# Performance work log

Hardware: AMD Instinct MI355X
Metric: run time of the kernel (lower is better)

The kernel has to match this reference:

```python
import jax, jax.numpy as jnp
import numpy as np


def setup_inputs() -> dict:
    key = jax.random.key(0)
    ks = jax.random.split(key, 6)
    B, N, d = 4096, 32768, 512
    return {
        "X_src": jax.random.normal(ks[0], (B, d), dtype=jnp.float32),
        "X_trans": jax.random.normal(ks[1], (B, d), dtype=jnp.float32),
        "Y_tgt": jax.random.normal(ks[2], (B, d), dtype=jnp.float32),
        "Z_src": jax.random.normal(ks[3], (N, d), dtype=jnp.float32),
        "Z_trans": jax.random.normal(ks[4], (N, d), dtype=jnp.float32),
        "Z_tgt": jax.random.normal(ks[5], (N, d), dtype=jnp.float32),
        "knn": 10,
    }


def _getknn(sc, k):
    # torch: topk(10) indices[:, :k], gather, sum  ==  sum of top-k values per row
    vals, _ = jax.lax.top_k(sc, k)  # [rows, k]
    return vals.sum() / k


def reference(X_src, X_trans, Y_tgt, Z_src, Z_trans, Z_tgt, knn):
    B = X_src.shape[0]
    f = 2.0 * (X_trans * Y_tgt).sum()
    # sc0: [B, N] similarity of translated src words vs target vocab
    fk0 = _getknn(X_trans @ Z_tgt.T, knn)
    # Z_trans.mm(Y_tgt.t()).t() == Y_tgt @ Z_trans.T : [B, N]
    fk1 = _getknn(Y_tgt @ Z_trans.T, knn)
    f = f - fk0 - fk1
    return -f / B
```

## Files before the change

kernel.cpp:

```cpp
#include <hip/hip_runtime.h>
#include <hip/hip_bf16.h>
#include <float.h>
#include <cstdint>


#define B_ROWS 4096
#define N_COLS 32768
#define D_K    512
#define BM     128
#define BN     128
#define BKT    64
#define NCHUNK (N_COLS / BN)
#define CSTRIDE 134

typedef __bf16 bf16x8 __attribute__((ext_vector_type(8)));
typedef float  f32x4  __attribute__((ext_vector_type(4)));
typedef unsigned short u16x2 __attribute__((ext_vector_type(2)));

__device__ __forceinline__ unsigned short f2bf(float f) {
    unsigned int u = __float_as_uint(f);
    u += 0x7FFFu + ((u >> 16) & 1u);
    return (unsigned short)(u >> 16);
}
__device__ __forceinline__ unsigned short f2sort(float f) {
    unsigned int x = f2bf(f);
    return (unsigned short)(x ^ (0x8000u | ((x >> 15) * 0x7FFFu)));
}
__device__ __forceinline__ float sort2f(unsigned int y) {
    unsigned int x = (y & 0x8000u) ? (y ^ 0x8000u) : (~y & 0xFFFFu);
    return __uint_as_float(x << 16);
}

__device__ __forceinline__ void gload_lds16(const void* g, void* l) {
    __builtin_amdgcn_global_load_lds(
        (const __attribute__((address_space(1))) unsigned int*)(uintptr_t)g,
        (__attribute__((address_space(3))) unsigned int*)(uintptr_t)l,
        16, 0, 0);
}

__global__ void zero_scalars(float* sc) {
    if (threadIdx.x < 3) sc[threadIdx.x] = 0.0f;
}

__global__ void prep_kernel(const float4* __restrict__ X,
                            const float4* __restrict__ Y,
                            const float4* __restrict__ Zt,
                            const float4* __restrict__ Ztr,
                            ushort4* __restrict__ A0, ushort4* __restrict__ A1,
                            ushort4* __restrict__ B0, ushort4* __restrict__ B1,
                            float* __restrict__ dotacc) {
    const int z = blockIdx.y;
    int i = blockIdx.x * 256 + threadIdx.x;
    const int stride = gridDim.x * 256;
    if (z == 0) {
        float s = 0.0f;
        for (; i < B_ROWS * D_K / 4; i += stride) {
            float4 x = X[i], y = Y[i];
            ushort4 u; u.x = f2bf(x.x); u.y = f2bf(x.y);
            u.z = f2bf(x.z); u.w = f2bf(x.w);
            A0[i] = u;
            s += x.x * y.x + x.y * y.y + x.z * y.z + x.w * y.w;
        }
        for (int o = 32; o > 0; o >>= 1) s += __shfl_down(s, o);
        __shared__ float wsum[4];
        int lane = threadIdx.x & 63, w = threadIdx.x >> 6;
        if (lane == 0) wsum[w] = s;
        __syncthreads();
        if (threadIdx.x == 0)
            atomicAdd(dotacc, wsum[0] + wsum[1] + wsum[2] + wsum[3]);
    } else {
        const float4* src = (z == 1) ? Y : (z == 2) ? Zt : Ztr;
        ushort4* dst = (z == 1) ? A1 : (z == 2) ? B0 : B1;
        int n4 = (z == 1) ? (B_ROWS * D_K / 4) : (N_COLS * D_K / 4);
        for (; i < n4; i += stride) {
            float4 f = src[i];
            ushort4 u; u.x = f2bf(f.x); u.y = f2bf(f.y);
            u.z = f2bf(f.z); u.w = f2bf(f.w);
            dst[i] = u;
        }
    }
}

__global__ __launch_bounds__(256, 4)
void gemm_topk_kernel(const unsigned short* __restrict__ A0g,
                      const unsigned short* __restrict__ A1g,
                      const unsigned short* __restrict__ B0g,
                      const unsigned short* __restrict__ B1g,
                      uint2* __restrict__ P0, uint2* __restrict__ P1) {
    const unsigned short* A  = blockIdx.y ? A1g : A0g;
    const unsigned short* Bm = blockIdx.y ? B1g : B0g;
    uint2* P2 = blockIdx.y ? P1 : P0;

    __shared__ __align__(128) unsigned short smem[BM * CSTRIDE];
    unsigned short* Alds = smem;
    unsigned short* Blds = smem + 16 * 512;

    const int tid  = threadIdx.x;
    const int lane = tid & 63;
    const int w    = tid >> 6;
    const int wm   = w >> 1;
    const int wn   = w & 1;
    const int quad = lane >> 4;
    const int mrow = lane & 15;

    const int b      = blockIdx.x;
    const int xcd    = b & 7;
    const int ii     = b >> 3;
    const int cw     = ii & 15;
    const int rowblk = (ii >> 4) & 31;
    const int cg     = ii >> 9;
    const int bn     = xcd * 32 + cg * 16 + cw;
    const int row0   = rowblk * BM;
    const int col0   = bn * BN;

    const unsigned short* gA[4];
    const unsigned short* gB[4];
    #pragma unroll
    for (int c = 0; c < 4; ++c) {
        int s  = w * 4 + c;
        int r  = (s >> 1) * 16 + mrow;
        int kc = (s & 1) * 32 + quad * 8;
        gA[c] = A  + (size_t)(row0 + r) * D_K + kc;
        gB[c] = Bm + (size_t)(col0 + r) * D_K + kc;
    }

    f32x4 acc[4][4];
    #pragma unroll
    for (int mi = 0; mi < 4; ++mi)
        #pragma unroll
        for (int ni = 0; ni < 4; ++ni)
            acc[mi][ni] = (f32x4){0.f, 0.f, 0.f, 0.f};

    for (int kt = 0; kt < D_K; kt += BKT) {
        #pragma unroll
        for (int c = 0; c < 4; ++c) {
            int s = w * 4 + c;
            gload_lds16(gA[c] + kt, Alds + s * 512);
            gload_lds16(gB[c] + kt, Blds + s * 512);
        }
        __syncthreads();
        #pragma unroll
        for (int kk32 = 0; kk32 < 2; ++kk32) {
            bf16x8 af[4], bfr[4];
            #pragma unroll
            for (int mi = 0; mi < 4; ++mi)
                af[mi] = *(const bf16x8*)(Alds + ((wm * 4 + mi) * 2 + kk32) * 512 + lane * 8);
            #pragma unroll
            for (int ni = 0; ni < 4; ++ni)
                bfr[ni] = *(const bf16x8*)(Blds + ((wn * 4 + ni) * 2 + kk32) * 512 + lane * 8);
            #pragma unroll
            for (int mi = 0; mi < 4; ++mi)
                #pragma unroll
                for (int ni = 0; ni < 4; ++ni)
                    acc[mi][ni] = __builtin_amdgcn_mfma_f32_16x16x32_bf16(
                        af[mi], bfr[ni], acc[mi][ni], 0, 0, 0);
        }
        __syncthreads();
    }

    unsigned short* Cs = smem;
    #pragma unroll
    for (int mi = 0; mi < 4; ++mi) {
        int r = wm * 64 + mi * 16 + quad * 4;
        #pragma unroll
        for (int ni = 0; ni < 4; ++ni) {
            int cc = wn * 64 + ni * 16 + mrow;
            #pragma unroll
            for (int reg = 0; reg < 4; ++reg)
                Cs[(r + reg) * CSTRIDE + cc] = f2sort(acc[mi][ni][reg]);
        }
    }
    __syncthreads();

    const int row  = w * 32 + (lane >> 1);
    const int half = lane & 1;
    const u16x2* rp = (const u16x2*)(Cs + row * CSTRIDE + half * 64);
    u16x2 t[4];
    #pragma unroll
    for (int i = 0; i < 4; ++i) t[i] = (u16x2){0, 0};
    #pragma unroll 8
    for (int j = 0; j < 32; ++j) {
        u16x2 v = rp[j];
        #pragma unroll
        for (int i = 0; i < 4; ++i) {
            u16x2 hi = __builtin_elementwise_max(t[i], v);
            v = __builtin_elementwise_min(t[i], v);
            t[i] = hi;
        }
    }
    unsigned int m0 = max((unsigned int)t[0].x, (unsigned int)t[3].y);
    unsigned int m1 = max((unsigned int)t[1].x, (unsigned int)t[2].y);
    unsigned int m2 = max((unsigned int)t[2].x, (unsigned int)t[1].y);
    unsigned int m3 = max((unsigned int)t[3].x, (unsigned int)t[0].y);
    uint2 outv = make_uint2(m0 | (m1 << 16), m2 | (m3 << 16));
    P2[((size_t)(row0 + row) * NCHUNK + bn) * 2 + half] = outv;
}

__global__ __launch_bounds__(256, 4)
void merge_topk_kernel(const unsigned int* __restrict__ P0,
                       const unsigned int* __restrict__ P1,
                       float* __restrict__ sc) {
    const int g    = blockIdx.y;
    const int lane = threadIdx.x & 63;
    const int w    = threadIdx.x >> 6;
    const int row  = blockIdx.x * 4 + w;
    const unsigned int* Rp = (g ? P1 : P0) + (size_t)row * (NCHUNK * 4);

    u16x2 t[10];
    #pragma unroll
    for (int i = 0; i < 10; ++i) t[i] = (u16x2){0, 0};
    #pragma unroll 4
    for (int it = 0; it < 16; ++it) {
        unsigned int raw = Rp[lane + 64 * it];
        u16x2 v = *(u16x2*)&raw;
        #pragma unroll
        for (int i = 0; i < 10; ++i) {
            u16x2 hi = __builtin_elementwise_max(t[i], v);
            v = __builtin_elementwise_min(t[i], v);
            t[i] = hi;
        }
    }
    unsigned int wreg[10];
    #pragma unroll
    for (int i = 0; i < 10; ++i) {
        unsigned int mv = max((unsigned int)t[i].x,
                              (unsigned int)t[9 - i].y);
        wreg[i] = (mv << 16) | ((unsigned int)lane << 4) | (unsigned int)i;
    }
    float sum10 = 0.0f;
    #pragma unroll
    for (int iter = 0; iter < 10; ++iter) {
        unsigned int mx = wreg[0];
        #pragma unroll
        for (int s = 1; s < 10; ++s) mx = max(mx, wreg[s]);
        #pragma unroll
        for (int o = 32; o > 0; o >>= 1)
            mx = max(mx, (unsigned int)__shfl_xor((int)mx, o));
        sum10 += sort2f(mx >> 16);
        #pragma unroll
        for (int s = 0; s < 10; ++s)
            if (wreg[s] == mx) wreg[s] = 0u;
    }
    if (lane == 0) atomicAdd(sc + 1 + g, sum10);
}

__global__ void finalize_kernel(const float* __restrict__ sc,
                                float* __restrict__ out) {
    if (threadIdx.x == 0) {
        float f = (sc[1] * 0.1f + sc[2] * 0.1f - 2.0f * sc[0]) * (1.0f / 4096.0f);
        out[0] = f;
    }
}

extern "C" void kernel_launch(void* const* d_in, const int* in_sizes, int n_in,
                              void* d_out, int out_size, void* d_ws, size_t ws_size,
                              hipStream_t stream) {
    const float* X_trans = (const float*)d_in[1];
    const float* Y_tgt   = (const float*)d_in[2];
    const float* Z_trans = (const float*)d_in[4];
    const float* Z_tgt   = (const float*)d_in[5];

    char* ws = (char*)d_ws;
    float* sc = (float*)ws;
    unsigned short* A0 = (unsigned short*)(ws + 256);
    unsigned short* A1 = A0 + (size_t)B_ROWS * D_K;
    unsigned short* B0 = A1 + (size_t)B_ROWS * D_K;
    unsigned short* B1 = B0 + (size_t)N_COLS * D_K;
    uint2* P0 = (uint2*)(B1 + (size_t)N_COLS * D_K);
    uint2* P1 = P0 + (size_t)B_ROWS * NCHUNK * 2;

    zero_scalars<<<1, 64, 0, stream>>>(sc);

    dim3 pgrid(2048, 4);
    prep_kernel<<<pgrid, 256, 0, stream>>>(
        (const float4*)X_trans, (const float4*)Y_tgt,
        (const float4*)Z_tgt, (const float4*)Z_trans,
        (ushort4*)A0, (ushort4*)A1, (ushort4*)B0, (ushort4*)B1, sc + 0);

    dim3 ggrid(8192, 2);
    gemm_topk_kernel<<<ggrid, 256, 0, stream>>>(A0, A1, B0, B1, P0, P1);

    dim3 mgrid(B_ROWS / 4, 2);
    merge_topk_kernel<<<mgrid, 256, 0, stream>>>(
        (const unsigned int*)P0, (const unsigned int*)P1, sc);

    finalize_kernel<<<1, 64, 0, stream>>>(sc, (float*)d_out);
}
```

Baseline: 797.7 us.

## Enlarge GEMM tiles to 256x256 with 4-stage LDS pipeline and register top-k

```diff
diff --git a/kernel.cpp b/kernel.cpp
--- a/kernel.cpp
+++ b/kernel.cpp
@@ -7,11 +7,7 @@
 #define B_ROWS 4096
 #define N_COLS 32768
 #define D_K    512
-#define BM     128
-#define BN     128
-#define BKT    64
-#define NCHUNK (N_COLS / BN)
-#define CSTRIDE 134
+#define NCHUNK (N_COLS / 128)
 
 typedef __bf16 bf16x8 __attribute__((ext_vector_type(8)));
 typedef float  f32x4  __attribute__((ext_vector_type(4)));
@@ -22,14 +18,17 @@
     u += 0x7FFFu + ((u >> 16) & 1u);
     return (unsigned short)(u >> 16);
 }
-__device__ __forceinline__ unsigned short f2sort(float f) {
-    unsigned int x = f2bf(f);
-    return (unsigned short)(x ^ (0x8000u | ((x >> 15) * 0x7FFFu)));
+__device__ __forceinline__ unsigned f2sort32(float f) {
+    unsigned u = __float_as_uint(f);
+    u += 0x7FFFu + ((u >> 16) & 1u);
+    return u ^ (0x80000000u | (unsigned)((int)u >> 31));
 }
 __device__ __forceinline__ float sort2f(unsigned int y) {
     unsigned int x = (y & 0x8000u) ? (y ^ 0x8000u) : (~y & 0xFFFFu);
     return __uint_as_float(x << 16);
 }
+__device__ __forceinline__ unsigned umax(unsigned a, unsigned b) { return a > b ? a : b; }
+__device__ __forceinline__ unsigned umin(unsigned a, unsigned b) { return a < b ? a : b; }
 
 __device__ __forceinline__ void gload_lds16(const void* g, void* l) {
     __builtin_amdgcn_global_load_lds(
@@ -81,7 +80,54 @@
     }
 }
 
-__global__ __launch_bounds__(256, 4)
+#define BARRIER()  asm volatile("s_barrier" ::: "memory")
+#define VMCNT(N)   asm volatile("s_waitcnt vmcnt(" #N ")" ::: "memory")
+#define LGKM(N)    asm volatile("s_waitcnt lgkmcnt(" #N ")" ::: "memory")
+#define MEMFENCE() asm volatile("" ::: "memory")
+
+#define STAGE(T) do { \
+    gload_lds16(gA0 + (T) * 32, smem + ((T) & 3) * 16384 + w * 512); \
+    gload_lds16(gA1 + (T) * 32, smem + ((T) & 3) * 16384 + (8 + w) * 512); \
+    gload_lds16(gB0 + (T) * 32, smem + ((T) & 3) * 16384 + 8192 + w * 512); \
+    gload_lds16(gB1 + (T) * 32, smem + ((T) & 3) * 16384 + 8192 + (8 + w) * 512); \
+} while (0)
+
+#define LOAD_AF(ARR, SLOT) { _Pragma("unroll") for (int mi = 0; mi < 8; ++mi) \
+    ARR[mi] = *(const bf16x8*)(smem + (SLOT) * 16384 + abase + mi * 512 + lane8); }
+
+#define MFMA32(ARR) { __builtin_amdgcn_s_setprio(1); \
+    _Pragma("unroll") for (int mi = 0; mi < 8; ++mi) { \
+    _Pragma("unroll") for (int ni = 0; ni < 4; ++ni) { \
+        acc[mi][ni] = __builtin_amdgcn_mfma_f32_16x16x32_bf16( \
+            bfr[ni], ARR[mi], acc[mi][ni], 0, 0, 0); } } \
+    __builtin_amdgcn_s_setprio(0); }
+
+#define KSTEP(J) do { \
+    bf16x8 bfr[4]; \
+    _Pragma("unroll") for (int ni = 0; ni < 4; ++ni) \
+        bfr[ni] = *(const bf16x8*)(smem + ((J) & 3) * 16384 + bbase + ni * 512 + lane8); \
+    MEMFENCE(); \
+    if ((J) & 1) { \
+        if ((J) < 15) LOAD_AF(af0, ((J) + 1) & 3) \
+        MFMA32(af1) \
+    } else { \
+        if ((J) < 15) LOAD_AF(af1, ((J) + 1) & 3) \
+        MFMA32(af0) \
+    } \
+    if ((J) < 12)       { LGKM(8); BARRIER(); STAGE((J) + 4); VMCNT(8); BARRIER(); } \
+    else if ((J) == 12) { VMCNT(4); BARRIER(); } \
+    else if ((J) == 13) { VMCNT(0); BARRIER(); } \
+} while (0)
+
+#define CSWAP(a, b) { unsigned _hi = umax(a, b), _lo = umin(a, b); a = _hi; b = _lo; }
+#define SORT4() { CSWAP(m0, m1); CSWAP(m2, m3); CSWAP(m0, m2); CSWAP(m1, m3); CSWAP(m1, m2); }
+#define INS(V) { u16x2 _hi; \
+    _hi = __builtin_elementwise_max(t0, V); V = __builtin_elementwise_min(t0, V); t0 = _hi; \
+    _hi = __builtin_elementwise_max(t1, V); V = __builtin_elementwise_min(t1, V); t1 = _hi; \
+    _hi = __builtin_elementwise_max(t2, V); V = __builtin_elementwise_min(t2, V); t2 = _hi; \
+    _hi = __builtin_elementwise_max(t3, V); V = __builtin_elementwise_min(t3, V); t3 = _hi; }
+
+__global__ __launch_bounds__(512, 2)
 void gemm_topk_kernel(const unsigned short* __restrict__ A0g,
                       const unsigned short* __restrict__ A1g,
                       const unsigned short* __restrict__ B0g,
@@ -91,109 +137,98 @@
     const unsigned short* Bm = blockIdx.y ? B1g : B0g;
     uint2* P2 = blockIdx.y ? P1 : P0;
 
-    __shared__ __align__(128) unsigned short smem[BM * CSTRIDE];
-    unsigned short* Alds = smem;
-    unsigned short* Blds = smem + 16 * 512;
-
-    const int tid  = threadIdx.x;
-    const int lane = tid & 63;
-    const int w    = tid >> 6;
-    const int wm   = w >> 1;
-    const int wn   = w & 1;
-    const int quad = lane >> 4;
-    const int mrow = lane & 15;
+    __shared__ __align__(128) unsigned short smem[4 * 16384];
+
+    const int tid   = threadIdx.x;
+    const int lane  = tid & 63;
+    const int w     = tid >> 6;
+    const int wm    = w >> 2;
+    const int wn    = w & 3;
+    const int quad  = lane >> 4;
+    const int mrow  = lane & 15;
+    const int lane8 = lane * 8;
 
     const int b      = blockIdx.x;
     const int xcd    = b & 7;
     const int ii     = b >> 3;
-    const int cw     = ii & 15;
-    const int rowblk = (ii >> 4) & 31;
-    const int cg     = ii >> 9;
-    const int bn     = xcd * 32 + cg * 16 + cw;
-    const int row0   = rowblk * BM;
-    const int col0   = bn * BN;
-
-    const unsigned short* gA[4];
-    const unsigned short* gB[4];
-    #pragma unroll
-    for (int c = 0; c < 4; ++c) {
-        int s  = w * 4 + c;
-        int r  = (s >> 1) * 16 + mrow;
-        int kc = (s & 1) * 32 + quad * 8;
-        gA[c] = A  + (size_t)(row0 + r) * D_K + kc;
-        gB[c] = Bm + (size_t)(col0 + r) * D_K + kc;
-    }
-
-    f32x4 acc[4][4];
-    #pragma unroll
-    for (int mi = 0; mi < 4; ++mi)
+    const int cw     = ii & 7;
+    const int rowblk = (ii >> 3) & 15;
+    const int cg     = ii >> 7;
+    const int bn     = xcd * 16 + cg * 8 + cw;
+    const int row0   = rowblk * 256;
+    const int col0   = bn * 256;
+
+    const unsigned short* gA0 = A  + (size_t)(row0 + w * 16 + mrow) * D_K + quad * 8;
+    const unsigned short* gA1 = gA0 + 128 * D_K;
+    const unsigned short* gB0 = Bm + (size_t)(col0 + w * 16 + mrow) * D_K + quad * 8;
+    const unsigned short* gB1 = gB0 + 128 * D_K;
+
+    const int abase = wm * 4096;
+    const int bbase = 8192 + wn * 2048;
+
+    f32x4 acc[8][4];
+    #pragma unroll
+    for (int mi = 0; mi < 8; ++mi)
         #pragma unroll
         for (int ni = 0; ni < 4; ++ni)
             acc[mi][ni] = (f32x4){0.f, 0.f, 0.f, 0.f};
 
-    for (int kt = 0; kt < D_K; kt += BKT) {
-        #pragma unroll
-        for (int c = 0; c < 4; ++c) {
-            int s = w * 4 + c;
-            gload_lds16(gA[c] + kt, Alds + s * 512);
-            gload_lds16(gB[c] + kt, Blds + s * 512);
-        }
-        __syncthreads();
-        #pragma unroll
-        for (int kk32 = 0; kk32 < 2; ++kk32) {
-            bf16x8 af[4], bfr[4];
-            #pragma unroll
-            for (int mi = 0; mi < 4; ++mi)
-                af[mi] = *(const bf16x8*)(Alds + ((wm * 4 + mi) * 2 + kk32) * 512 + lane * 8);
-            #pragma unroll
-            for (int ni = 0; ni < 4; ++ni)
-                bfr[ni] = *(const bf16x8*)(Blds + ((wn * 4 + ni) * 2 + kk32) * 512 + lane * 8);
-            #pragma unroll
-            for (int mi = 0; mi < 4; ++mi)
-                #pragma unroll
-                for (int ni = 0; ni < 4; ++ni)
-                    acc[mi][ni] = __builtin_amdgcn_mfma_f32_16x16x32_bf16(
-                        af[mi], bfr[ni], acc[mi][ni], 0, 0, 0);
-        }
-        __syncthreads();
-    }
-
-    unsigned short* Cs = smem;
-    #pragma unroll
-    for (int mi = 0; mi < 4; ++mi) {
-        int r = wm * 64 + mi * 16 + quad * 4;
+    bf16x8 af0[8], af1[8];
+
+    STAGE(0); MEMFENCE();
+    STAGE(1); MEMFENCE();
+    STAGE(2); MEMFENCE();
+    STAGE(3);
+    VMCNT(8);
+    BARRIER();
+    LOAD_AF(af0, 0)
+
+    KSTEP(0);  KSTEP(1);  KSTEP(2);  KSTEP(3);
+    KSTEP(4);  KSTEP(5);  KSTEP(6);  KSTEP(7);
+    KSTEP(8);  KSTEP(9);  KSTEP(10); KSTEP(11);
+    KSTEP(12); KSTEP(13); KSTEP(14); KSTEP(15);
+
+    const int chunk = bn * 2 + (wn >> 1);
+    const int half  = wn & 1;
+    #pragma unroll
+    for (int mi = 0; mi < 8; ++mi) {
+        u16x2 t0 = {0, 0}, t1 = {0, 0}, t2 = {0, 0}, t3 = {0, 0};
         #pragma unroll
         for (int ni = 0; ni < 4; ++ni) {
-            int cc = wn * 64 + ni * 16 + mrow;
-            #pragma unroll
-            for (int reg = 0; reg < 4; ++reg)
-                Cs[(r + reg) * CSTRIDE + cc] = f2sort(acc[mi][ni][reg]);
-        }
-    }
-    __syncthreads();
-
-    const int row  = w * 32 + (lane >> 1);
-    const int half = lane & 1;
-    const u16x2* rp = (const u16x2*)(Cs + row * CSTRIDE + half * 64);
-    u16x2 t[4];
-    #pragma unroll
-    for (int i = 0; i < 4; ++i) t[i] = (u16x2){0, 0};
-    #pragma unroll 8
-    for (int j = 0; j < 32; ++j) {
-        u16x2 v = rp[j];
-        #pragma unroll
-        for (int i = 0; i < 4; ++i) {
-            u16x2 hi = __builtin_elementwise_max(t[i], v);
-            v = __builtin_elementwise_min(t[i], v);
-            t[i] = hi;
-        }
-    }
-    unsigned int m0 = max((unsigned int)t[0].x, (unsigned int)t[3].y);
-    unsigned int m1 = max((unsigned int)t[1].x, (unsigned int)t[2].y);
-    unsigned int m2 = max((unsigned int)t[2].x, (unsigned int)t[1].y);
-    unsigned int m3 = max((unsigned int)t[3].x, (unsigned int)t[0].y);
-    uint2 outv = make_uint2(m0 | (m1 << 16), m2 | (m3 << 16));
-    P2[((size_t)(row0 + row) * NCHUNK + bn) * 2 + half] = outv;
+            unsigned s0 = f2sort32(acc[mi][ni][0]);
+            unsigned s1 = f2sort32(acc[mi][ni][1]);
+            unsigned s2 = f2sort32(acc[mi][ni][2]);
+            unsigned s3 = f2sort32(acc[mi][ni][3]);
+            unsigned pa = (s0 >> 16) | (s1 & 0xFFFF0000u);
+            unsigned pb = (s2 >> 16) | (s3 & 0xFFFF0000u);
+            u16x2 v0 = *(u16x2*)&pa;
+            u16x2 v1 = *(u16x2*)&pb;
+            INS(v0); INS(v1);
+        }
+        unsigned m0 = umax((unsigned)t0.x, (unsigned)t3.y);
+        unsigned m1 = umax((unsigned)t1.x, (unsigned)t2.y);
+        unsigned m2 = umax((unsigned)t2.x, (unsigned)t1.y);
+        unsigned m3 = umax((unsigned)t3.x, (unsigned)t0.y);
+        SORT4();
+        #pragma unroll
+        for (int st = 0; st < 2; ++st) {
+            unsigned pa = m0 | (m1 << 16);
+            unsigned pb = m2 | (m3 << 16);
+            unsigned qa = (unsigned)__shfl_xor((int)pa, st ? 32 : 16);
+            unsigned qb = (unsigned)__shfl_xor((int)pb, st ? 32 : 16);
+            unsigned ra = (qa >> 16) | (qa << 16);
+            unsigned rb = (qb >> 16) | (qb << 16);
+            u16x2 n0 = __builtin_elementwise_max(*(u16x2*)&pa, *(u16x2*)&rb);
+            u16x2 n1 = __builtin_elementwise_max(*(u16x2*)&pb, *(u16x2*)&ra);
+            m0 = n0.x; m1 = n0.y; m2 = n1.x; m3 = n1.y;
+            SORT4();
+        }
+        if (quad == 0) {
+            int row_g = row0 + wm * 128 + mi * 16 + mrow;
+            P2[((size_t)row_g * NCHUNK + chunk) * 2 + half] =
+                make_uint2(m0 | (m1 << 16), m2 | (m3 << 16));
+        }
+    }
 }
 
 __global__ __launch_bounds__(256, 4)
@@ -223,8 +258,8 @@
     unsigned int wreg[10];
     #pragma unroll
     for (int i = 0; i < 10; ++i) {
-        unsigned int mv = max((unsigned int)t[i].x,
-                              (unsigned int)t[9 - i].y);
+        unsigned int mv = umax((unsigned int)t[i].x,
+                               (unsigned int)t[9 - i].y);
         wreg[i] = (mv << 16) | ((unsigned int)lane << 4) | (unsigned int)i;
     }
     float sum10 = 0.0f;
@@ -232,10 +267,10 @@
     for (int iter = 0; iter < 10; ++iter) {
         unsigned int mx = wreg[0];
         #pragma unroll
-        for (int s = 1; s < 10; ++s) mx = max(mx, wreg[s]);
+        for (int s = 1; s < 10; ++s) mx = umax(mx, wreg[s]);
         #pragma unroll
         for (int o = 32; o > 0; o >>= 1)
-            mx = max(mx, (unsigned int)__shfl_xor((int)mx, o));
+            mx = umax(mx, (unsigned int)__shfl_xor((int)mx, o));
         sum10 += sort2f(mx >> 16);
         #pragma unroll
         for (int s = 0; s < 10; ++s)
@@ -277,8 +312,8 @@
         (const float4*)Z_tgt, (const float4*)Z_trans,
         (ushort4*)A0, (ushort4*)A1, (ushort4*)B0, (ushort4*)B1, sc + 0);
 
-    dim3 ggrid(8192, 2);
-    gemm_topk_kernel<<<ggrid, 256, 0, stream>>>(A0, A1, B0, B1, P0, P1);
+    dim3 ggrid(2048, 2);
+    gemm_topk_kernel<<<ggrid, 512, 0, stream>>>(A0, A1, B0, B1, P0, P1);
 
     dim3 mgrid(B_ROWS / 4, 2);
     merge_topk_kernel<<<mgrid, 256, 0, stream>>>(
```

After: 683.5 us. 1.17x faster.
